# Performance work log

Hardware: AMD Instinct MI355X
Metric: run time of the kernel (lower is better)

Reference implementation:

```python
import jax, jax.numpy as jnp
import numpy as np
import math

D_MODEL = 2048
N_HEADS = 16
D_HEAD = D_MODEL // N_HEADS
MAX_T = 2048
B, T = 2, 2048


def rotate_half(x):
    # interleaved rotate: (x0,x1,x2,x3,...) -> (-x1,x0,-x3,x2,...)
    x1 = x[..., ::2]
    x2 = x[..., 1::2]
    return jnp.stack((-x2, x1), axis=-1).reshape(x.shape)


def setup_inputs() -> dict:
    key = jax.random.key(0)
    k1, k2, k3 = jax.random.split(key, 3)
    x = jax.random.normal(k1, (B, T, D_MODEL), dtype=jnp.float32)
    # torch nn.Linear weights: [out, in]
    s = 1.0 / math.sqrt(D_MODEL)
    Wqkv = jax.random.uniform(k2, (3 * D_MODEL, D_MODEL), dtype=jnp.float32, minval=-s, maxval=s)
    WO = jax.random.uniform(k3, (D_MODEL, D_MODEL), dtype=jnp.float32, minval=-s, maxval=s)
    return {"x": x, "Wqkv": Wqkv, "WO": WO}


def reference(x, Wqkv, WO):
    Bx, Tx, _ = x.shape
    # RoPE tables (buffers)
    pos = jnp.arange(Tx, dtype=jnp.float32)
    freqs = jnp.exp(-math.log(10000.0) * jnp.arange(0, D_HEAD, 2, dtype=jnp.float32) / D_HEAD)
    angles = pos[:, None] * freqs[None, :]               # [T, d_head/2]
    sin = jnp.repeat(jnp.sin(angles), 2, axis=-1)        # [T, d_head]
    cos = jnp.repeat(jnp.cos(angles), 2, axis=-1)
    sin = sin[None, None, :, :]
    cos = cos[None, None, :, :]

    qkv = x @ Wqkv.T                                     # [B, T, 3D]
    q, k, v = jnp.split(qkv, 3, axis=-1)
    def to_heads(t):
        return t.reshape(Bx, Tx, N_HEADS, D_HEAD).transpose(0, 2, 1, 3)  # [B,H,T,d]
    q, k, v = to_heads(q), to_heads(k), to_heads(v)

    q = q * cos + rotate_half(q) * sin
    k = k * cos + rotate_half(k) * sin

    scores = jnp.einsum('bhqd,bhkd->bhqk', q, k) / math.sqrt(D_HEAD)
    mask = jnp.triu(jnp.full((Tx, Tx), -jnp.inf, dtype=scores.dtype), k=1)
    scores = scores + mask
    attn = jax.nn.softmax(scores, axis=-1)
    out = jnp.einsum('bhqk,bhkd->bhqd', attn, v)
    out = out.transpose(0, 2, 1, 3).reshape(Bx, Tx, D_MODEL)
    return out @ WO.T
```

## Files before the change

### kernel.cpp

```cpp
#include <hip/hip_runtime.h>
#include <hip/hip_bf16.h>

typedef unsigned short u16;
typedef __attribute__((ext_vector_type(8))) short bf16x8;
typedef __attribute__((ext_vector_type(4))) float f32x4;

#define B_   2
#define T_   2048
#define DM   2048
#define NH   16
#define DH   128
#define NQKV 6144

__device__ __forceinline__ u16 f2bf(float f) {
  __hip_bfloat16 h = __float2bfloat16(f);
  u16 u; __builtin_memcpy(&u, &h, 2); return u;
}
__device__ __forceinline__ float bf2f(u16 u) {
  __hip_bfloat16 h; __builtin_memcpy(&h, &u, 2); return __bfloat162float(h);
}
__device__ __forceinline__ void gl_lds16(const void* g, void* l) {
  __builtin_amdgcn_global_load_lds(
      (__attribute__((address_space(1))) unsigned int*)g,
      (__attribute__((address_space(3))) unsigned int*)l, 16, 0, 0);
}
__device__ __forceinline__ f32x4 MFMA(bf16x8 a, bf16x8 b, f32x4 c) {
  return __builtin_amdgcn_mfma_f32_16x16x32_bf16(a, b, c, 0, 0, 0);
}

__global__ __launch_bounds__(256) void cast_kernel(const float* __restrict__ in,
                                                   u16* __restrict__ out, int n4) {
  int i = blockIdx.x * 256 + threadIdx.x;
  if (i >= n4) return;
  float4 v = ((const float4*)in)[i];
  ushort4 o;
  o.x = f2bf(v.x); o.y = f2bf(v.y); o.z = f2bf(v.z); o.w = f2bf(v.w);
  ((ushort4*)out)[i] = o;
}

__global__ __launch_bounds__(256) void rope_tab(float2* __restrict__ tab) {
  int idx = blockIdx.x * 256 + threadIdx.x;
  if (idx >= T_ * 64) return;
  int t = idx >> 6, i = idx & 63;
  float freq = __expf(-9.210340371976184f * (float)i / 64.0f);
  float sn, cs;
  sincosf((float)t * freq, &sn, &cs);
  tab[idx] = make_float2(cs, sn);
}

#define G1_M 4096
#define G1_N 6144
#define G1_K 2048

#define MFMA_Q(AQ, M0)                                                        \
  _Pragma("unroll") for (int e_ = 0; e_ < 2; ++e_)                            \
  _Pragma("unroll") for (int n_ = 0; n_ < 4; ++n_)                            \
  _Pragma("unroll") for (int kb_ = 0; kb_ < 2; ++kb_)                         \
    acc[(M0) + e_][n_] = MFMA(AQ[e_][kb_], bfr[n_][kb_], acc[(M0) + e_][n_])

#define BARRIER() asm volatile("s_barrier" ::: "memory")
#define LGKM0()                                                               \
  do {                                                                        \
    asm volatile("s_waitcnt lgkmcnt(0)" ::: "memory");                        \
    __builtin_amdgcn_sched_barrier(0);                                        \
  } while (0)
#define SBAR() __builtin_amdgcn_sched_barrier(0)

__global__ __launch_bounds__(512, 2) void gemm1_8ph(const u16* __restrict__ A,
                                                    const u16* __restrict__ Bm,
                                                    const float2* __restrict__ tab,
                                                    u16* __restrict__ Qo,
                                                    u16* __restrict__ Ko,
                                                    u16* __restrict__ Vt) {
  __shared__ alignas(16) u16 As[2][256 * 64];
  __shared__ alignas(16) u16 Bs[2][256 * 64];
  const int tid = threadIdx.x;
  const int w = tid >> 6, lane = tid & 63;
  const int lrow = lane & 15, quad = lane >> 4;
  const long tileM = (long)blockIdx.y * 256, tileN = (long)blockIdx.x * 256;
  const int wm = (w >> 2) * 128, wn = (w & 3) * 64;

  const int sw8 = w * 8;
  const int srowL = lane >> 3;
  const int schunk = ((lane & 7) ^ srowL) * 8;
  const u16* Ag0 = A + (tileM + sw8 + srowL) * (long)G1_K + schunk;
  const u16* Bg0 = Bm + (tileN + sw8 + srowL) * (long)G1_K + schunk;

  auto stgA = [&](int tt, int h) {
    const int b = tt & 1;
    gl_lds16(Ag0 + (size_t)(h * 128) * G1_K + tt * 64,
             &As[b][(h * 128 + sw8) * 64]);
    gl_lds16(Ag0 + (size_t)(h * 128 + 64) * G1_K + tt * 64,
             &As[b][(h * 128 + 64 + sw8) * 64]);
  };
  auto stgB = [&](int tt, int h) {
    const int b = tt & 1;
    gl_lds16(Bg0 + (size_t)(h * 128) * G1_K + tt * 64,
             &Bs[b][(h * 128 + sw8) * 64]);
    gl_lds16(Bg0 + (size_t)(h * 128 + 64) * G1_K + tt * 64,
             &Bs[b][(h * 128 + 64 + sw8) * 64]);
  };

  const int aBase = (wm + lrow) * 64;
  const int bBase = (wn + lrow) * 64;
  const int slot[2] = { (quad ^ (lrow & 7)) * 8, ((4 + quad) ^ (lrow & 7)) * 8 };

  f32x4 acc[8][4] = {};
  bf16x8 bfr[4][2];
  bf16x8 aCur[2][2], aNxt[2][2];

  stgA(0, 0); stgA(0, 1); stgB(0, 0); stgB(0, 1);
  stgB(1, 0); stgB(1, 1); stgA(1, 0);
  asm volatile("s_waitcnt vmcnt(6)" ::: "memory");
  BARRIER();
#pragma unroll
  for (int ni = 0; ni < 4; ++ni)
#pragma unroll
    for (int kb = 0; kb < 2; ++kb)
      bfr[ni][kb] = *(const bf16x8*)(Bs[0] + bBase + ni * 1024 + slot[kb]);
#pragma unroll
  for (int e = 0; e < 2; ++e)
#pragma unroll
    for (int kb = 0; kb < 2; ++kb)
      aCur[e][kb] = *(const bf16x8*)(As[0] + aBase + e * 1024 + slot[kb]);

#pragma unroll 1
  for (int t = 0; t < 32; ++t) {
    const u16* AsC = As[t & 1];
    LGKM0();
    __builtin_amdgcn_s_setprio(1);
    MFMA_Q(aCur, 0);
    __builtin_amdgcn_s_setprio(0);
    SBAR();
#pragma unroll
    for (int e = 0; e < 2; ++e)
#pragma unroll
      for (int kb = 0; kb < 2; ++kb)
        aNxt[e][kb] = *(const bf16x8*)(AsC + aBase + (2 + e) * 1024 + slot[kb]);
    if (t + 1 < 32) stgA(t + 1, 1);
    BARRIER();
    LGKM0();
    __builtin_amdgcn_s_setprio(1);
    MFMA_Q(aNxt, 2);
    __builtin_amdgcn_s_setprio(0);
    SBAR();
#pragma unroll
    for (int e = 0; e < 2; ++e)
#pragma unroll
      for (int kb = 0; kb < 2; ++kb)
        aCur[e][kb] = *(const bf16x8*)(AsC + aBase + (4 + e) * 1024 + slot[kb]);
    if (t + 2 < 32) stgB(t + 2, 0);
    BARRIER();
    LGKM0();
    __builtin_amdgcn_s_setprio(1);
    MFMA_Q(aCur, 4);
    __builtin_amdgcn_s_setprio(0);
    SBAR();
#pragma unroll
    for (int e = 0; e < 2; ++e)
#pragma unroll
      for (int kb = 0; kb < 2; ++kb)
        aNxt[e][kb] = *(const bf16x8*)(AsC + aBase + (6 + e) * 1024 + slot[kb]);
    if (t + 2 < 32) stgB(t + 2, 1);
    if (t < 30) { asm volatile("s_waitcnt vmcnt(4)" ::: "memory"); }
    else       { asm volatile("s_waitcnt vmcnt(0)" ::: "memory"); }
    BARRIER();
    LGKM0();
    __builtin_amdgcn_s_setprio(1);
    MFMA_Q(aNxt, 6);
    __builtin_amdgcn_s_setprio(0);
    SBAR();
    if (t + 1 < 32) {
      const u16* AsN = As[(t + 1) & 1];
      const u16* BsN = Bs[(t + 1) & 1];
#pragma unroll
      for (int ni = 0; ni < 4; ++ni)
#pragma unroll
        for (int kb = 0; kb < 2; ++kb)
          bfr[ni][kb] = *(const bf16x8*)(BsN + bBase + ni * 1024 + slot[kb]);
#pragma unroll
      for (int e = 0; e < 2; ++e)
#pragma unroll
        for (int kb = 0; kb < 2; ++kb)
          aCur[e][kb] = *(const bf16x8*)(AsN + aBase + e * 1024 + slot[kb]);
    }
    if (t + 2 < 32) stgA(t + 2, 0);
    BARRIER();
  }

  const long crow = tileM + wm + quad * 4;
  const long ccol = tileN + wn + lrow;
  const int sec = (int)(tileN >> 11);
  const int bI = (int)(tileM >> 11);
  const int tG0 = (int)(tileM & 2047);
  if (sec < 2) {
    u16* dst = sec == 0 ? Qo : Ko;
    const float scale = sec == 0 ? 0.08838834764831845f : 1.0f;
#pragma unroll
    for (int ni = 0; ni < 4; ++ni) {
      const int col = (int)((ccol + ni * 16) & 2047);
      const int h = col >> 7, d = col & 127;
      const int i = d >> 1;
      const float2* tcol = tab + i;
#pragma unroll
      for (int mi = 0; mi < 8; ++mi) {
        const int rowL = wm + mi * 16 + quad * 4;
#pragma unroll
        for (int r = 0; r < 4; ++r) {
          const int tt = tG0 + rowL + r;
          float x = acc[mi][ni][r];
          float p = __shfl_xor(x, 1);
          float2 sc = tcol[(size_t)tt * 64];
          float o = (x * sc.x + ((d & 1) ? p : -p) * sc.y) * scale;
          dst[(((size_t)(bI * 16 + h)) * T_ + tt) * DH + d] = f2bf(o);
        }
      }
    }
  } else {
#pragma unroll
    for (int ni = 0; ni < 4; ++ni) {
      const int col = (int)((ccol + ni * 16) & 2047);
      const int h = col >> 7, d = col & 127;
#pragma unroll
      for (int mi = 0; mi < 8; ++mi) {
        const int t0 = tG0 + wm + mi * 16 + quad * 4;
        ushort4 v4;
        v4.x = f2bf(acc[mi][ni][0]);
        v4.y = f2bf(acc[mi][ni][1]);
        v4.z = f2bf(acc[mi][ni][2]);
        v4.w = f2bf(acc[mi][ni][3]);
        *(ushort4*)(Vt + (((size_t)(bI * 16 + h)) * DH + d) * (size_t)T_ + t0) = v4;
      }
    }
  }
}

__global__ __launch_bounds__(256) void gemm_bt(const u16* __restrict__ A,
                                               const u16* __restrict__ Bm,
                                               void* __restrict__ Cp,
                                               int M, int N, int K, int out_f32) {
  __shared__ u16 As[128 * 64];
  __shared__ u16 Bs[128 * 64];
  const int tid  = threadIdx.x;
  const int wave = tid >> 6, lane = tid & 63;
  const int lrow = lane & 15, quad = lane >> 4;
  const long tileM = (long)blockIdx.y * 128, tileN = (long)blockIdx.x * 128;
  const int wm = (wave >> 1) * 64, wn = (wave & 1) * 64;
  const int sRowIn = lane >> 3;
  const int sChunk = (lane & 7) ^ sRowIn;
  const int sRow0  = wave * 32 + sRowIn;
  const u16* Ag = A + (tileM + sRow0) * (long)K + sChunk * 8;
  const u16* Bg = Bm + (tileN + sRow0) * (long)K + sChunk * 8;
  u16* AsW = As + wave * 2048;
  u16* BsW = Bs + wave * 2048;
  f32x4 acc[4][4] = {};
  for (int kt = 0; kt < K; kt += 64) {
#pragma unroll
    for (int i = 0; i < 4; ++i)
      gl_lds16(Ag + kt + (size_t)i * 8 * K, AsW + i * 512);
#pragma unroll
    for (int i = 0; i < 4; ++i)
      gl_lds16(Bg + kt + (size_t)i * 8 * K, BsW + i * 512);
    __syncthreads();
#pragma unroll
    for (int kb = 0; kb < 2; ++kb) {
      const int slot8 = (((kb * 4 + quad) ^ (lrow & 7)) * 8);
      bf16x8 af[4], bfr[4];
#pragma unroll
      for (int i = 0; i < 4; ++i)
        af[i]  = *(const bf16x8*)(As + (wm + i * 16 + lrow) * 64 + slot8);
#pragma unroll
      for (int i = 0; i < 4; ++i)
        bfr[i] = *(const bf16x8*)(Bs + (wn + i * 16 + lrow) * 64 + slot8);
#pragma unroll
      for (int mi = 0; mi < 4; ++mi)
#pragma unroll
        for (int ni = 0; ni < 4; ++ni)
          acc[mi][ni] = MFMA(af[mi], bfr[ni], acc[mi][ni]);
    }
    __syncthreads();
  }
  const long crow = tileM + wm + quad * 4;
  const long ccol = tileN + wn + lrow;
  if (out_f32) {
    float* C = (float*)Cp;
#pragma unroll
    for (int mi = 0; mi < 4; ++mi)
#pragma unroll
      for (int ni = 0; ni < 4; ++ni)
#pragma unroll
        for (int r = 0; r < 4; ++r)
          C[(crow + mi * 16 + r) * (long)N + (ccol + ni * 16)] = acc[mi][ni][r];
  } else {
    u16* C = (u16*)Cp;
#pragma unroll
    for (int mi = 0; mi < 4; ++mi)
#pragma unroll
      for (int ni = 0; ni < 4; ++ni)
#pragma unroll
        for (int r = 0; r < 4; ++r)
          C[(crow + mi * 16 + r) * (long)N + (ccol + ni * 16)] = f2bf(acc[mi][ni][r]);
  }
}

__global__ __launch_bounds__(512) void attn_flash(const u16* __restrict__ Q,
                                                  const u16* __restrict__ K,
                                                  const u16* __restrict__ Vt,
                                                  u16* __restrict__ AO) {
  __shared__ u16 Kl[2][64 * 128];
  __shared__ u16 Vl[2][128 * 64];
  __shared__ u16 Pl[8 * 16 * 64];
  const int pairIdx = blockIdx.x;
  const int bh = blockIdx.y;
  const int b = bh >> 4, h = bh & 15;
  const int tid = threadIdx.x;
  const int wave = tid >> 6, lane = tid & 63;
  const int lrow = lane & 15, quad = lane >> 4;
  const u16* Qb = Q + (size_t)bh * T_ * DH;
  const u16* Kb = K + (size_t)bh * T_ * DH;
  const u16* Vb = Vt + (size_t)bh * DH * T_;

  const int kRowIn = lane >> 4;
  const int vRowIn = lane >> 3;
  const int vChunk = (lane & 7) ^ vRowIn;
  u16* PlW = Pl + wave * 1024;

  auto stageKV = [&](int j, int buf) {
#pragma unroll
    for (int i = 0; i < 2; ++i) {
      int krow = wave * 8 + i * 4 + kRowIn;
      int kch = (lane & 15) ^ (krow & 15);
      gl_lds16(Kb + (size_t)(j * 64 + krow) * DH + kch * 8,
               Kl[buf] + wave * 1024 + i * 512);
    }
#pragma unroll
    for (int i = 0; i < 2; ++i) {
      int vd = wave * 16 + i * 8 + vRowIn;
      gl_lds16(Vb + (size_t)vd * T_ + j * 64 + vChunk * 8,
               Vl[buf] + wave * 1024 + i * 512);
    }
  };

  for (int pass = 0; pass < 2; ++pass) {
    const int qt = pass == 0 ? (15 - pairIdx) : pairIdx;
    const int qbase = qt * 128;
    const int nkt = 2 * qt + 2;

    bf16x8 qf[4];
    {
      const u16* qrow = Qb + (size_t)(qbase + wave * 16 + lrow) * DH + quad * 8;
#pragma unroll
      for (int kc = 0; kc < 4; ++kc) qf[kc] = *(const bf16x8*)(qrow + kc * 32);
    }
    f32x4 o[8] = {};
    float lsum[4] = {0.f, 0.f, 0.f, 0.f};

    stageKV(0, 0);

    for (int j = 0; j < nkt; ++j) {
      const int cb = j & 1;
      if (j + 1 < nkt) {
        stageKV(j + 1, cb ^ 1);
        asm volatile("s_waitcnt vmcnt(4)" ::: "memory");
      } else {
        asm volatile("s_waitcnt vmcnt(0)" ::: "memory");
      }
      BARRIER();

      const u16* KlC = Kl[cb];
      const u16* VlC = Vl[cb];
      f32x4 s[4] = {};
#pragma unroll
      for (int kc = 0; kc < 4; ++kc)
#pragma unroll
        for (int ns = 0; ns < 4; ++ns) {
          bf16x8 kf = *(const bf16x8*)(KlC + (ns * 16 + lrow) * 128 +
                                       (((kc * 4 + quad) ^ lrow) * 8));
          s[ns] = MFMA(qf[kc], kf, s[ns]);
        }
      if (j >= 2 * qt) {
        const int jl = (j - 2 * qt) * 64;
#pragma unroll
        for (int ns = 0; ns < 4; ++ns)
#pragma unroll
          for (int r = 0; r < 4; ++r)
            if (jl + ns * 16 + lrow > wave * 16 + quad * 4 + r)
              s[ns][r] = -__builtin_inff();
      }
#pragma unroll
      for (int r = 0; r < 4; ++r) {
        const int prow = quad * 4 + r;
#pragma unroll
        for (int ns = 0; ns < 4; ++ns) {
          float p = __expf(s[ns][r]);
          PlW[prow * 64 + (((ns * 2 + (lrow >> 3)) ^ (prow & 7)) * 8) +
              (lrow & 7)] = f2bf(p);
          lsum[r] += p;
        }
      }

#pragma unroll
      for (int kc = 0; kc < 2; ++kc) {
        bf16x8 pf = *(const bf16x8*)(PlW + lrow * 64 +
                                     (((kc * 4 + quad) ^ (lrow & 7)) * 8));
#pragma unroll
        for (int os = 0; os < 8; ++os) {
          bf16x8 vf = *(const bf16x8*)(VlC + (os * 16 + lrow) * 64 +
                                       (((kc * 4 + quad) ^ (lrow & 7)) * 8));
          o[os] = MFMA(pf, vf, o[os]);
        }
      }
      asm volatile("s_waitcnt lgkmcnt(0)" ::: "memory");
      BARRIER();
    }
#pragma unroll
    for (int r = 0; r < 4; ++r) {
      lsum[r] += __shfl_xor(lsum[r], 1, 16);
      lsum[r] += __shfl_xor(lsum[r], 2, 16);
      lsum[r] += __shfl_xor(lsum[r], 4, 16);
      lsum[r] += __shfl_xor(lsum[r], 8, 16);
    }
#pragma unroll
    for (int r = 0; r < 4; ++r) {
      float inv = 1.0f / lsum[r];
      const size_t row = (size_t)b * T_ + qbase + wave * 16 + quad * 4 + r;
      u16* dst = AO + row * DM + h * DH;
#pragma unroll
      for (int os = 0; os < 8; ++os) dst[os * 16 + lrow] = f2bf(o[os][r] * inv);
    }
  }
}

extern "C" void kernel_launch(void* const* d_in, const int* in_sizes, int n_in,
                              void* d_out, int out_size, void* d_ws, size_t ws_size,
                              hipStream_t stream) {
  const float* x    = (const float*)d_in[0];
  const float* Wqkv = (const float*)d_in[1];
  const float* WO   = (const float*)d_in[2];
  char* ws = (char*)d_ws;
  size_t off = 0;
  u16* xb   = (u16*)(ws + off); off += (size_t)B_ * T_ * DM * 2;
  u16* wqb  = (u16*)(ws + off); off += (size_t)NQKV * DM * 2;
  u16* wob  = (u16*)(ws + off); off += (size_t)DM * DM * 2;
  u16* Qb   = (u16*)(ws + off); off += (size_t)B_ * NH * T_ * DH * 2;
  u16* Kb   = (u16*)(ws + off); off += (size_t)B_ * NH * T_ * DH * 2;
  u16* Vtb  = (u16*)(ws + off); off += (size_t)B_ * NH * T_ * DH * 2;
  float2* tabp = (float2*)(ws + off); off += (size_t)T_ * 64 * 8;
  u16* AO   = xb;

  rope_tab<<<(T_ * 64 + 255) / 256, 256, 0, stream>>>(tabp);
  cast_kernel<<<(B_ * T_ * DM / 4 + 255) / 256, 256, 0, stream>>>(x, xb, B_ * T_ * DM / 4);
  cast_kernel<<<(NQKV * DM / 4 + 255) / 256, 256, 0, stream>>>(Wqkv, wqb, NQKV * DM / 4);
  cast_kernel<<<(DM * DM / 4 + 255) / 256, 256, 0, stream>>>(WO, wob, DM * DM / 4);

  gemm1_8ph<<<dim3(G1_N / 256, G1_M / 256), 512, 0, stream>>>(xb, wqb, tabp,
                                                              Qb, Kb, Vtb);

  attn_flash<<<dim3(8, B_ * NH), 512, 0, stream>>>(Qb, Kb, Vtb, AO);

  gemm_bt<<<dim3(DM / 128, B_ * T_ / 128), 256, 0, stream>>>(
      AO, wob, d_out, B_ * T_, DM, DM, 1);
}
```

Before: 370.1 us.

## Give each attention wave 32 query rows and merge the three cast kernels

The attention kernel drops from 8 waves of 16 query rows to 4 waves of 32 query rows, so each K and V fragment read from LDS feeds two MFMAs. This halves LDS fragment traffic per unit of compute and doubles the loads each thread issues to stage K and V. The three fp32-to-bf16 cast launches are also merged into one kernel that picks its source by index. The price is more registers per thread and fewer waves per block to hide latency, since the grid stays at 256 blocks.

```diff
diff --git a/kernel.cpp b/kernel.cpp
--- a/kernel.cpp
+++ b/kernel.cpp
@@ -28,14 +28,23 @@
   return __builtin_amdgcn_mfma_f32_16x16x32_bf16(a, b, c, 0, 0, 0);
 }
 
-__global__ __launch_bounds__(256) void cast_kernel(const float* __restrict__ in,
-                                                   u16* __restrict__ out, int n4) {
+__global__ __launch_bounds__(256) void cast3(const float* __restrict__ x,
+                                             u16* __restrict__ xb,
+                                             const float* __restrict__ wq,
+                                             u16* __restrict__ wqb,
+                                             const float* __restrict__ wo,
+                                             u16* __restrict__ wob) {
+  const int n1 = B_ * T_ * DM / 4, n2 = NQKV * DM / 4, n3 = DM * DM / 4;
   int i = blockIdx.x * 256 + threadIdx.x;
-  if (i >= n4) return;
-  float4 v = ((const float4*)in)[i];
+  const float4* src; ushort4* dst; int k;
+  if (i < n1)           { src = (const float4*)x;  dst = (ushort4*)xb;  k = i; }
+  else if (i < n1 + n2) { src = (const float4*)wq; dst = (ushort4*)wqb; k = i - n1; }
+  else if (i < n1 + n2 + n3) { src = (const float4*)wo; dst = (ushort4*)wob; k = i - n1 - n2; }
+  else return;
+  float4 v = src[k];
   ushort4 o;
   o.x = f2bf(v.x); o.y = f2bf(v.y); o.z = f2bf(v.z); o.w = f2bf(v.w);
-  ((ushort4*)out)[i] = o;
+  dst[k] = o;
 }
 
 __global__ __launch_bounds__(256) void rope_tab(float2* __restrict__ tab) {
@@ -303,13 +312,13 @@
   }
 }
 
-__global__ __launch_bounds__(512) void attn_flash(const u16* __restrict__ Q,
+__global__ __launch_bounds__(256) void attn_flash(const u16* __restrict__ Q,
                                                   const u16* __restrict__ K,
                                                   const u16* __restrict__ Vt,
                                                   u16* __restrict__ AO) {
   __shared__ u16 Kl[2][64 * 128];
   __shared__ u16 Vl[2][128 * 64];
-  __shared__ u16 Pl[8 * 16 * 64];
+  __shared__ u16 Pl[4 * 32 * 64];
   const int pairIdx = blockIdx.x;
   const int bh = blockIdx.y;
   const int b = bh >> 4, h = bh & 15;
@@ -323,21 +332,21 @@
   const int kRowIn = lane >> 4;
   const int vRowIn = lane >> 3;
   const int vChunk = (lane & 7) ^ vRowIn;
-  u16* PlW = Pl + wave * 1024;
+  u16* PlW = Pl + wave * 2048;
 
   auto stageKV = [&](int j, int buf) {
 #pragma unroll
-    for (int i = 0; i < 2; ++i) {
-      int krow = wave * 8 + i * 4 + kRowIn;
+    for (int i = 0; i < 4; ++i) {
+      int krow = wave * 16 + i * 4 + kRowIn;
       int kch = (lane & 15) ^ (krow & 15);
       gl_lds16(Kb + (size_t)(j * 64 + krow) * DH + kch * 8,
-               Kl[buf] + wave * 1024 + i * 512);
-    }
-#pragma unroll
-    for (int i = 0; i < 2; ++i) {
-      int vd = wave * 16 + i * 8 + vRowIn;
+               Kl[buf] + wave * 2048 + i * 512);
+    }
+#pragma unroll
+    for (int i = 0; i < 4; ++i) {
+      int vd = wave * 32 + i * 8 + vRowIn;
       gl_lds16(Vb + (size_t)vd * T_ + j * 64 + vChunk * 8,
-               Vl[buf] + wave * 1024 + i * 512);
+               Vl[buf] + wave * 2048 + i * 512);
     }
   };
 
@@ -346,14 +355,16 @@
     const int qbase = qt * 128;
     const int nkt = 2 * qt + 2;
 
-    bf16x8 qf[4];
-    {
-      const u16* qrow = Qb + (size_t)(qbase + wave * 16 + lrow) * DH + quad * 8;
-#pragma unroll
-      for (int kc = 0; kc < 4; ++kc) qf[kc] = *(const bf16x8*)(qrow + kc * 32);
-    }
-    f32x4 o[8] = {};
-    float lsum[4] = {0.f, 0.f, 0.f, 0.f};
+    bf16x8 qf[2][4];
+#pragma unroll
+    for (int m = 0; m < 2; ++m) {
+      const u16* qrow =
+          Qb + (size_t)(qbase + wave * 32 + m * 16 + lrow) * DH + quad * 8;
+#pragma unroll
+      for (int kc = 0; kc < 4; ++kc) qf[m][kc] = *(const bf16x8*)(qrow + kc * 32);
+    }
+    f32x4 o[2][8] = {};
+    float lsum[2][4] = {};
 
     stageKV(0, 0);
 
@@ -361,7 +372,7 @@
       const int cb = j & 1;
       if (j + 1 < nkt) {
         stageKV(j + 1, cb ^ 1);
-        asm volatile("s_waitcnt vmcnt(4)" ::: "memory");
+        asm volatile("s_waitcnt vmcnt(8)" ::: "memory");
       } else {
         asm volatile("s_waitcnt vmcnt(0)" ::: "memory");
       }
@@ -369,64 +380,75 @@
 
       const u16* KlC = Kl[cb];
       const u16* VlC = Vl[cb];
-      f32x4 s[4] = {};
+      f32x4 s[2][4] = {};
 #pragma unroll
       for (int kc = 0; kc < 4; ++kc)
 #pragma unroll
         for (int ns = 0; ns < 4; ++ns) {
           bf16x8 kf = *(const bf16x8*)(KlC + (ns * 16 + lrow) * 128 +
                                        (((kc * 4 + quad) ^ lrow) * 8));
-          s[ns] = MFMA(qf[kc], kf, s[ns]);
+          s[0][ns] = MFMA(qf[0][kc], kf, s[0][ns]);
+          s[1][ns] = MFMA(qf[1][kc], kf, s[1][ns]);
         }
       if (j >= 2 * qt) {
         const int jl = (j - 2 * qt) * 64;
 #pragma unroll
-        for (int ns = 0; ns < 4; ++ns)
-#pragma unroll
-          for (int r = 0; r < 4; ++r)
-            if (jl + ns * 16 + lrow > wave * 16 + quad * 4 + r)
-              s[ns][r] = -__builtin_inff();
-      }
-#pragma unroll
-      for (int r = 0; r < 4; ++r) {
-        const int prow = quad * 4 + r;
-#pragma unroll
-        for (int ns = 0; ns < 4; ++ns) {
-          float p = __expf(s[ns][r]);
-          PlW[prow * 64 + (((ns * 2 + (lrow >> 3)) ^ (prow & 7)) * 8) +
-              (lrow & 7)] = f2bf(p);
-          lsum[r] += p;
+        for (int m = 0; m < 2; ++m)
+#pragma unroll
+          for (int ns = 0; ns < 4; ++ns)
+#pragma unroll
+            for (int r = 0; r < 4; ++r)
+              if (jl + ns * 16 + lrow > wave * 32 + m * 16 + quad * 4 + r)
+                s[m][ns][r] = -__builtin_inff();
+      }
+#pragma unroll
+      for (int m = 0; m < 2; ++m)
+#pragma unroll
+        for (int r = 0; r < 4; ++r) {
+          const int prow = m * 16 + quad * 4 + r;
+#pragma unroll
+          for (int ns = 0; ns < 4; ++ns) {
+            float p = __expf(s[m][ns][r]);
+            PlW[prow * 64 + (((ns * 2 + (lrow >> 3)) ^ (prow & 7)) * 8) +
+                (lrow & 7)] = f2bf(p);
+            lsum[m][r] += p;
+          }
         }
-      }
 
 #pragma unroll
       for (int kc = 0; kc < 2; ++kc) {
-        bf16x8 pf = *(const bf16x8*)(PlW + lrow * 64 +
-                                     (((kc * 4 + quad) ^ (lrow & 7)) * 8));
+        const int sl = ((kc * 4 + quad) ^ (lrow & 7)) * 8;
+        bf16x8 pf0 = *(const bf16x8*)(PlW + lrow * 64 + sl);
+        bf16x8 pf1 = *(const bf16x8*)(PlW + (16 + lrow) * 64 + sl);
 #pragma unroll
         for (int os = 0; os < 8; ++os) {
-          bf16x8 vf = *(const bf16x8*)(VlC + (os * 16 + lrow) * 64 +
-                                       (((kc * 4 + quad) ^ (lrow & 7)) * 8));
-          o[os] = MFMA(pf, vf, o[os]);
+          bf16x8 vf = *(const bf16x8*)(VlC + (os * 16 + lrow) * 64 + sl);
+          o[0][os] = MFMA(pf0, vf, o[0][os]);
+          o[1][os] = MFMA(pf1, vf, o[1][os]);
         }
       }
       asm volatile("s_waitcnt lgkmcnt(0)" ::: "memory");
       BARRIER();
     }
 #pragma unroll
-    for (int r = 0; r < 4; ++r) {
-      lsum[r] += __shfl_xor(lsum[r], 1, 16);
-      lsum[r] += __shfl_xor(lsum[r], 2, 16);
-      lsum[r] += __shfl_xor(lsum[r], 4, 16);
-      lsum[r] += __shfl_xor(lsum[r], 8, 16);
-    }
-#pragma unroll
-    for (int r = 0; r < 4; ++r) {
-      float inv = 1.0f / lsum[r];
-      const size_t row = (size_t)b * T_ + qbase + wave * 16 + quad * 4 + r;
-      u16* dst = AO + row * DM + h * DH;
-#pragma unroll
-      for (int os = 0; os < 8; ++os) dst[os * 16 + lrow] = f2bf(o[os][r] * inv);
+    for (int m = 0; m < 2; ++m) {
+#pragma unroll
+      for (int r = 0; r < 4; ++r) {
+        lsum[m][r] += __shfl_xor(lsum[m][r], 1, 16);
+        lsum[m][r] += __shfl_xor(lsum[m][r], 2, 16);
+        lsum[m][r] += __shfl_xor(lsum[m][r], 4, 16);
+        lsum[m][r] += __shfl_xor(lsum[m][r], 8, 16);
+      }
+#pragma unroll
+      for (int r = 0; r < 4; ++r) {
+        float inv = 1.0f / lsum[m][r];
+        const size_t row =
+            (size_t)b * T_ + qbase + wave * 32 + m * 16 + quad * 4 + r;
+        u16* dst = AO + row * DM + h * DH;
+#pragma unroll
+        for (int os = 0; os < 8; ++os)
+          dst[os * 16 + lrow] = f2bf(o[m][os][r] * inv);
+      }
     }
   }
 }
@@ -449,14 +471,13 @@
   u16* AO   = xb;
 
   rope_tab<<<(T_ * 64 + 255) / 256, 256, 0, stream>>>(tabp);
-  cast_kernel<<<(B_ * T_ * DM / 4 + 255) / 256, 256, 0, stream>>>(x, xb, B_ * T_ * DM / 4);
-  cast_kernel<<<(NQKV * DM / 4 + 255) / 256, 256, 0, stream>>>(Wqkv, wqb, NQKV * DM / 4);
-  cast_kernel<<<(DM * DM / 4 + 255) / 256, 256, 0, stream>>>(WO, wob, DM * DM / 4);
+  const int nc = (B_ * T_ * DM + NQKV * DM + DM * DM) / 4;
+  cast3<<<(nc + 255) / 256, 256, 0, stream>>>(x, xb, Wqkv, wqb, WO, wob);
 
   gemm1_8ph<<<dim3(G1_N / 256, G1_M / 256), 512, 0, stream>>>(xb, wqb, tabp,
                                                               Qb, Kb, Vtb);
 
-  attn_flash<<<dim3(8, B_ * NH), 512, 0, stream>>>(Qb, Kb, Vtb, AO);
+  attn_flash<<<dim3(8, B_ * NH), 256, 0, stream>>>(Qb, Kb, Vtb, AO);
 
   gemm_bt<<<dim3(DM / 128, B_ * T_ / 128), 256, 0, stream>>>(
       AO, wob, d_out, B_ * T_, DM, DM, 1);
```

Result: slower. 385.0 us (+4.0%).
